# Kernel optimization log

Measured on AMD Instinct MI355X. Metric: run time of the kernel, lower is better.

## Reference

```python
import math
import jax, jax.numpy as jnp
import numpy as np

MODEL_DIM = 4096
NUM_EXPERTS = 16
COMP_PER_EXP = 4
PROJ_DIM = 4
TOTAL_COMP = NUM_EXPERTS * COMP_PER_EXP
B = 8192
K = 2
CAPACITY_FACTOR = 1.0
MIN_CAPACITY = 8
LOG2PI = math.log(2.0 * math.pi)


def setup_inputs() -> dict:
    key = jax.random.key(0)
    ks = jax.random.split(key, 4)
    input = jax.random.normal(ks[0], (B, MODEL_DIM), dtype=jnp.float32)
    # drop_centers mask (bernoulli over uniform prior ~ 1/64 each); deterministic all-false here
    drop_mask = jnp.zeros((TOTAL_COMP,), dtype=bool)
    means = jax.random.normal(ks[1], (TOTAL_COMP, PROJ_DIM), dtype=jnp.float32) / math.sqrt(PROJ_DIM)
    log_vars = jnp.full((TOTAL_COMP, PROJ_DIM), 4.0, dtype=jnp.float32)
    mix_logits = jnp.zeros((TOTAL_COMP,), dtype=jnp.float32)
    W_down = jax.random.normal(ks[2], (MODEL_DIM, PROJ_DIM), dtype=jnp.float32) / math.sqrt(MODEL_DIM)
    W_up = jax.random.normal(ks[3], (PROJ_DIM, MODEL_DIM), dtype=jnp.float32) / math.sqrt(PROJ_DIM)
    return {"input": input, "drop_mask": drop_mask, "means": means, "log_vars": log_vars,
            "mix_logits": mix_logits, "W_down": W_down, "W_up": W_up}


def top2gating(logits, capacity_factor, min_capacity):
    S, E = logits.shape
    gates = jax.nn.softmax(logits, axis=1)
    org_gates = gates
    idx1 = jnp.argmax(gates, axis=1)
    mask1 = jax.nn.one_hot(idx1, E, dtype=jnp.int32)
    logits_ex1 = jnp.where(mask1.astype(bool), -jnp.inf, logits)
    idx2 = jnp.argmax(logits_ex1, axis=1)
    mask2 = jax.nn.one_hot(idx2, E, dtype=jnp.int32)
    loc1 = jnp.cumsum(mask1, axis=0) - 1
    loc2 = jnp.cumsum(mask2, axis=0) - 1 + jnp.sum(mask1, axis=0, keepdims=True)
    exp_counts = jnp.sum(mask1 + mask2, axis=0)
    # _capacity: ceil(tokens/experts * 2*cf), floored at min_capacity (static)
    capacity = max(int(math.ceil(S / E * capacity_factor * 2.0)), min_capacity)
    mask1 = mask1 * (loc1 < capacity).astype(jnp.int32)
    mask2 = mask2 * (loc2 < capacity).astype(jnp.int32)
    loc1_s = jnp.sum(loc1 * mask1, axis=1)
    loc2_s = jnp.sum(loc2 * mask2, axis=1)
    m1f = mask1.astype(gates.dtype)
    m2f = mask2.astype(gates.dtype)
    g1 = jnp.sum(gates * m1f, axis=1)
    g2 = jnp.sum(gates * m2f, axis=1)
    denom = jnp.maximum(g1 + g2, jnp.finfo(gates.dtype).eps)
    g1 = g1 / denom
    g2 = g2 / denom
    oh1 = jax.nn.one_hot(loc1_s, capacity, dtype=gates.dtype)  # [S, C]
    oh2 = jax.nn.one_hot(loc2_s, capacity, dtype=gates.dtype)
    combine = (jnp.einsum('s,se,sc->sec', g1, m1f, oh1)
               + jnp.einsum('s,se,sc->sec', g2, m2f, oh2))
    dispatch = combine.astype(bool)
    return combine, dispatch, exp_counts, org_gates


def reference(input, drop_mask, means, log_vars, mix_logits, W_down, W_up):
    x = jax.lax.stop_gradient(input)
    # Down_Projector: linear down / up with reconstruction loss
    proj = x @ W_down                      # [B, P]
    recon = proj @ W_up                    # [B, D]
    recover_loss = jnp.mean((recon - x) ** 2)
    z = jax.lax.stop_gradient(proj)        # projected_input.detach()
    # GMM component log-likelihoods (diagonal covariance)
    diff = z[:, None, :] - means[None, :, :]           # [B, TC, P]
    vars_ = jnp.exp(log_vars)                          # [TC, P]
    mdist = jnp.sum(diff * diff / (vars_ + 1e-6), axis=-1)  # [B, TC]
    log_det = jnp.sum(log_vars, axis=-1)               # [TC]
    comp_logits = -0.5 * (mdist + log_det + PROJ_DIM * LOG2PI)
    gmm_logits = comp_logits + jax.nn.log_softmax(mix_logits)[None, :]
    gmm_logits = jnp.where(drop_mask[None, :], -jnp.inf, gmm_logits)
    posterior = jax.nn.softmax(gmm_logits, axis=-1)
    expert_post = jnp.max(posterior.reshape(-1, NUM_EXPERTS, COMP_PER_EXP), axis=2)  # [B, E]
    nll = -jnp.mean(jax.scipy.special.logsumexp(gmm_logits, axis=1))
    # sum of rolls for k=2
    expert_logits = expert_post + jnp.roll(expert_post, 1, axis=-1)
    combine, dispatch, exp_counts, org_gates = top2gating(
        jax.lax.stop_gradient(expert_logits), CAPACITY_FACTOR, MIN_CAPACITY)
    return (nll + recover_loss, combine, dispatch, exp_counts, org_gates)
```

## Files before the change

kernel.cpp:

```cpp
#include <hip/hip_runtime.h>
#include <math.h>

#define NTOK 8192
#define MD   4096
#define NE   16
#define CAP  1024
static __device__ const float LOG2PI_F = 1.8378770664093453f;

typedef float vf4 __attribute__((ext_vector_type(4)));

#define OFF_COMB 1ull
#define OFF_DISP (OFF_COMB + (size_t)NTOK * NE * CAP)
#define OFF_CNT  (OFF_DISP + (size_t)NTOK * NE * CAP)
#define OFF_ORG  (OFF_CNT + NE)
#define FILL_FLOATS ((size_t)OFF_ORG)
#define FILL_F4     (FILL_FLOATS / 4)
#define FILL_TAIL   (FILL_F4 * 4)

#define NBLK     2048
#define TOKBLK   512
#define CHUNK_F4 16384ull
#define NCHUNK   ((int)((FILL_F4 + CHUNK_F4 - 1) / CHUNK_F4))

__global__ __launch_bounds__(256) void kfused(
    const float* __restrict__ x, const float* __restrict__ means,
    const float* __restrict__ logv, const float* __restrict__ mix,
    const float* __restrict__ Wd, const float* __restrict__ Wu,
    float* __restrict__ out,
    int* __restrict__ e1w, int* __restrict__ e2w,
    float* __restrict__ g1w, float* __restrict__ g2w,
    float* __restrict__ nllp, float* __restrict__ recp,
    float4* __restrict__ pw, int* __restrict__ qctr)
{
    const int b    = blockIdx.x;
    const int tid  = threadIdx.x;
    const int lane = tid & 63;
    const int wave = tid >> 6;

    if (b < TOKBLK) {
        float* org_out = out + OFF_ORG;
        float4 mu = *reinterpret_cast<const float4*>(means + lane * 4);
        float4 lv = *reinterpret_cast<const float4*>(logv + lane * 4);
        const float logdet = lv.x + lv.y + lv.z + lv.w;
        const float iv0 = 1.f / (expf(lv.x) + 1e-6f);
        const float iv1 = 1.f / (expf(lv.y) + 1e-6f);
        const float iv2 = 1.f / (expf(lv.z) + 1e-6f);
        const float iv3 = 1.f / (expf(lv.w) + 1e-6f);
        float mz = mix[lane];
        float mmax = mz;
#pragma unroll
        for (int m = 32; m; m >>= 1) mmax = fmaxf(mmax, __shfl_xor(mmax, m));
        float msum = expf(mz - mmax);
#pragma unroll
        for (int m = 32; m; m >>= 1) msum += __shfl_xor(msum, m);
        const float cbase = -0.5f * (logdet + 4.0f * LOG2PI_F)
                          + (mz - (mmax + logf(msum)));

        for (int rep = 0; rep < 4; ++rep) {
            const int t = (b * 4 + wave) * 4 + rep;
            const float* xrow = x + (size_t)t * MD;

            float p0 = 0.f, p1 = 0.f, p2 = 0.f, p3 = 0.f;
            float r0 = 0.f, r1 = 0.f, r2 = 0.f, r3 = 0.f;
            float xn = 0.f;
#pragma unroll 4
            for (int j = 0; j < 16; ++j) {
                const int d0 = (j * 64 + lane) * 4;
                float4 v = *reinterpret_cast<const float4*>(xrow + d0);
                float4 w0 = *reinterpret_cast<const float4*>(Wd + (size_t)d0 * 4);
                float4 w1 = *reinterpret_cast<const float4*>(Wd + (size_t)(d0 + 1) * 4);
                float4 w2 = *reinterpret_cast<const float4*>(Wd + (size_t)(d0 + 2) * 4);
                float4 w3 = *reinterpret_cast<const float4*>(Wd + (size_t)(d0 + 3) * 4);
                p0 += v.x * w0.x + v.y * w1.x + v.z * w2.x + v.w * w3.x;
                p1 += v.x * w0.y + v.y * w1.y + v.z * w2.y + v.w * w3.y;
                p2 += v.x * w0.z + v.y * w1.z + v.z * w2.z + v.w * w3.z;
                p3 += v.x * w0.w + v.y * w1.w + v.z * w2.w + v.w * w3.w;
                float4 u0 = *reinterpret_cast<const float4*>(Wu + d0);
                float4 u1 = *reinterpret_cast<const float4*>(Wu + MD + d0);
                float4 u2 = *reinterpret_cast<const float4*>(Wu + 2 * MD + d0);
                float4 u3 = *reinterpret_cast<const float4*>(Wu + 3 * MD + d0);
                r0 += v.x * u0.x + v.y * u0.y + v.z * u0.z + v.w * u0.w;
                r1 += v.x * u1.x + v.y * u1.y + v.z * u1.z + v.w * u1.w;
                r2 += v.x * u2.x + v.y * u2.y + v.z * u2.z + v.w * u2.w;
                r3 += v.x * u3.x + v.y * u3.y + v.z * u3.z + v.w * u3.w;
                xn += v.x * v.x + v.y * v.y + v.z * v.z + v.w * v.w;
            }
#pragma unroll
            for (int m = 32; m; m >>= 1) {
                p0 += __shfl_xor(p0, m); p1 += __shfl_xor(p1, m);
                p2 += __shfl_xor(p2, m); p3 += __shfl_xor(p3, m);
                r0 += __shfl_xor(r0, m); r1 += __shfl_xor(r1, m);
                r2 += __shfl_xor(r2, m); r3 += __shfl_xor(r3, m);
                xn += __shfl_xor(xn, m);
            }

            if (lane == 0) {
                recp[t] = xn - 2.f * (p0 * r0 + p1 * r1 + p2 * r2 + p3 * r3);
                float4 pv; pv.x = p0; pv.y = p1; pv.z = p2; pv.w = p3;
                pw[t] = pv;
            }

            float dd, mdist;
            dd = p0 - mu.x; mdist  = dd * dd * iv0;
            dd = p1 - mu.y; mdist += dd * dd * iv1;
            dd = p2 - mu.z; mdist += dd * dd * iv2;
            dd = p3 - mu.w; mdist += dd * dd * iv3;
            float gl = -0.5f * mdist + cbase;

            float gmax = gl;
#pragma unroll
            for (int m = 32; m; m >>= 1) gmax = fmaxf(gmax, __shfl_xor(gmax, m));
            float gsum = expf(gl - gmax);
#pragma unroll
            for (int m = 32; m; m >>= 1) gsum += __shfl_xor(gsum, m);
            float lse = gmax + logf(gsum);
            if (lane == 0) nllp[t] = lse;
            float post = expf(gl - lse);

            float q = post;
            q = fmaxf(q, __shfl_xor(q, 1));
            q = fmaxf(q, __shfl_xor(q, 2));
            float ep = __shfl(q, (lane * 4) & 63);
            float epm1 = __shfl(ep, (lane + 15) & 15);
            float el = ep + epm1;

            float m16 = el;
#pragma unroll
            for (int m = 8; m; m >>= 1) m16 = fmaxf(m16, __shfl_xor(m16, m, 16));
            float ex = expf(el - m16);
            float s16 = ex;
#pragma unroll
            for (int m = 8; m; m >>= 1) s16 += __shfl_xor(s16, m, 16);
            float gate = ex / s16;

            float bv = gate; int bi = lane & 15;
#pragma unroll
            for (int m = 8; m; m >>= 1) {
                float ov = __shfl_xor(bv, m, 16); int oi = __shfl_xor(bi, m, 16);
                if (ov > bv || (ov == bv && oi < bi)) { bv = ov; bi = oi; }
            }
            int i1 = bi;
            float el2 = ((lane & 15) == i1) ? -INFINITY : el;
            float bv2 = el2; int bi2 = lane & 15;
#pragma unroll
            for (int m = 8; m; m >>= 1) {
                float ov = __shfl_xor(bv2, m, 16); int oi = __shfl_xor(bi2, m, 16);
                if (ov > bv2 || (ov == bv2 && oi < bi2)) { bv2 = ov; bi2 = oi; }
            }
            int i2 = bi2;
            float g1 = __shfl(gate, i1, 16);
            float g2 = __shfl(gate, i2, 16);

            if (lane < 16) org_out[(size_t)t * 16 + lane] = gate;
            if (lane == 0) { e1w[t] = i1; e2w[t] = i2; g1w[t] = g1; g2w[t] = g2; }
        }
    }

    {
        vf4 z = (vf4)(0.f);
        vf4* o4 = reinterpret_cast<vf4*>(out);
        for (;;) {
            int c = atomicAdd(qctr, 1);
            if (c >= NCHUNK) break;
            size_t base = (size_t)c * CHUNK_F4;
            size_t end  = base + CHUNK_F4;
            if (end > FILL_F4) end = FILL_F4;
            for (size_t i = base + tid; i < end; i += 256)
                __builtin_nontemporal_store(z, o4 + i);
        }
    }
    if (b == 0 && tid == 0) out[FILL_TAIL] = 0.f;
}

__global__ __launch_bounds__(256) void krank(
    const int* __restrict__ e1, const int* __restrict__ e2,
    int* __restrict__ loc1, int* __restrict__ rank2,
    int* __restrict__ cnt1, int* __restrict__ cnt2)
{
    const int e = blockIdx.x & 15;
    const bool second = blockIdx.x >= 16;
    const int* keys = second ? e2 : e1;
    int* outloc = second ? rank2 : loc1;
    __shared__ int wtot[4];
    const int tid = threadIdx.x;
    const int w = tid >> 6, l = tid & 63;

    int kreg[32];
#pragma unroll
    for (int k = 0; k < 32; ++k) kreg[k] = keys[k * 256 + tid];

    int running = 0;
#pragma unroll
    for (int k = 0; k < 32; ++k) {
        bool pred = (kreg[k] == e);
        unsigned long long mask = __ballot(pred);
        int rin = __popcll(mask & ((1ull << l) - 1ull));
        if (l == 0) wtot[w] = __popcll(mask);
        __syncthreads();
        int off = 0;
        for (int i = 0; i < w; ++i) off += wtot[i];
        if (pred) outloc[k * 256 + tid] = running + off + rin;
        running += wtot[0] + wtot[1] + wtot[2] + wtot[3];
        __syncthreads();
    }
    if (tid == 0) { if (second) cnt2[e] = running; else cnt1[e] = running; }
}

__global__ __launch_bounds__(256) void kfinal(
    const int* __restrict__ e1w, const int* __restrict__ e2w,
    const float* __restrict__ g1w, const float* __restrict__ g2w,
    const int* __restrict__ loc1w, const int* __restrict__ rank2w,
    const int* __restrict__ cnt1, const int* __restrict__ cnt2,
    const float* __restrict__ nllp, const float* __restrict__ recp,
    const float4* __restrict__ pw, const float* __restrict__ Wu,
    float* __restrict__ out)
{
    if (blockIdx.x == 32) {
        const int tid = threadIdx.x;
        const int w = tid >> 6, lane = tid & 63;
        float v[22];
#pragma unroll
        for (int q = 0; q < 22; ++q) v[q] = 0.f;
        for (int t = tid; t < NTOK; t += 256) {
            v[0] += nllp[t];
            v[1] += recp[t];
            float4 p = pw[t];
            v[2] += p.x * p.x; v[3] += p.x * p.y; v[4] += p.x * p.z; v[5] += p.x * p.w;
            v[6] += p.y * p.y; v[7] += p.y * p.z; v[8] += p.y * p.w;
            v[9] += p.z * p.z; v[10] += p.z * p.w; v[11] += p.w * p.w;
        }
        for (int d = tid; d < MD; d += 256) {
            float u0 = Wu[d], u1 = Wu[MD + d], u2 = Wu[2 * MD + d], u3 = Wu[3 * MD + d];
            v[12] += u0 * u0; v[13] += u0 * u1; v[14] += u0 * u2; v[15] += u0 * u3;
            v[16] += u1 * u1; v[17] += u1 * u2; v[18] += u1 * u3;
            v[19] += u2 * u2; v[20] += u2 * u3; v[21] += u3 * u3;
        }
        __shared__ float part[22][4];
#pragma unroll
        for (int q = 0; q < 22; ++q) {
            float s = v[q];
#pragma unroll
            for (int m = 32; m; m >>= 1) s += __shfl_xor(s, m);
            if (lane == 0) part[q][w] = s;
        }
        __syncthreads();
        if (tid == 0) {
            float r[22];
#pragma unroll
            for (int q = 0; q < 22; ++q)
                r[q] = part[q][0] + part[q][1] + part[q][2] + part[q][3];
            float gs = r[2] * r[12] + r[6] * r[16] + r[9] * r[19] + r[11] * r[21]
                     + 2.f * (r[3] * r[13] + r[4] * r[14] + r[5] * r[15]
                            + r[7] * r[17] + r[8] * r[18] + r[10] * r[20]);
            out[0] = (-r[0] / (float)NTOK)
                   + (r[1] + gs) / ((float)NTOK * (float)MD);
        }
        return;
    }

    if (blockIdx.x == 0 && threadIdx.x < NE)
        out[OFF_CNT + threadIdx.x] = (float)(cnt1[threadIdx.x] + cnt2[threadIdx.x]);

    const int t = blockIdx.x * 256 + threadIdx.x;
    const int e1 = e1w[t], e2 = e2w[t];
    const int l1 = loc1w[t];
    const int l2 = rank2w[t] + cnt1[e2];
    float g1 = g1w[t], g2 = g2w[t];
    const bool m1 = l1 < CAP, m2 = l2 < CAP;
    g1 = m1 ? g1 : 0.f;
    g2 = m2 ? g2 : 0.f;
    float denom = fmaxf(g1 + g2, 1.1920929e-07f);
    g1 /= denom; g2 /= denom;
    float* comb = out + OFF_COMB;
    float* disp = out + OFF_DISP;
    if (m1) {
        size_t idx = (size_t)t * (NE * CAP) + (size_t)e1 * CAP + l1;
        comb[idx] = g1;
        disp[idx] = (g1 != 0.f) ? 1.f : 0.f;
    }
    if (m2) {
        size_t idx = (size_t)t * (NE * CAP) + (size_t)e2 * CAP + l2;
        comb[idx] = g2;
        disp[idx] = (g2 != 0.f) ? 1.f : 0.f;
    }
}

extern "C" void kernel_launch(void* const* d_in, const int* in_sizes, int n_in,
                              void* d_out, int out_size, void* d_ws, size_t ws_size,
                              hipStream_t stream) {
    const float* x     = (const float*)d_in[0];
    const float* means = (const float*)d_in[2];
    const float* logv  = (const float*)d_in[3];
    const float* mix   = (const float*)d_in[4];
    const float* Wd    = (const float*)d_in[5];
    const float* Wu    = (const float*)d_in[6];
    float* out = (float*)d_out;

    int*   qctr  = (int*)d_ws;
    int*   e1w   = qctr + 4;
    int*   e2w   = e1w + NTOK;
    float* g1w   = (float*)(e2w + NTOK);
    float* g2w   = g1w + NTOK;
    int*   loc1  = (int*)(g2w + NTOK);
    int*   rank2 = loc1 + NTOK;
    int*   cnt1  = rank2 + NTOK;
    int*   cnt2  = cnt1 + NE;
    float* nllp  = (float*)(cnt2 + NE);
    float* recp  = nllp + NTOK;
    float4* pw   = (float4*)(recp + NTOK);

    hipMemsetAsync(qctr, 0, sizeof(int), stream);
    kfused<<<NBLK, 256, 0, stream>>>(x, means, logv, mix, Wd, Wu, out,
                                     e1w, e2w, g1w, g2w, nllp, recp, pw, qctr);
    krank<<<32, 256, 0, stream>>>(e1w, e2w, loc1, rank2, cnt1, cnt2);
    kfinal<<<33, 256, 0, stream>>>(e1w, e2w, g1w, g2w, loc1, rank2, cnt1, cnt2,
                                   nllp, recp, pw, Wu, out);
}
```

Measured before the change: 192.1 us.

## Overlap part of the zero-fill with the rank kernel to hide its latency

The large zero-fill of the combine and dispatch outputs is split in two. Most of it stays in the fused gating kernel, and a reserved 64 MiB tail is cleared by extra blocks added to the rank kernel, so that fill overlaps the serial 32-block ranking work that would otherwise leave the GPU mostly idle. The fill chunk size is also halved for finer load balancing. This costs one extra counter and more blocks in the rank launch, and those blocks compete for bandwidth with the ranking blocks.

```diff
diff --git a/kernel.cpp b/kernel.cpp
--- a/kernel.cpp
+++ b/kernel.cpp
@@ -17,10 +17,14 @@
 #define FILL_F4     (FILL_FLOATS / 4)
 #define FILL_TAIL   (FILL_F4 * 4)
 
+#define RESERVE_F4  4194304ull
+#define MAIN_F4     (FILL_F4 - RESERVE_F4)
+
 #define NBLK     2048
 #define TOKBLK   512
-#define CHUNK_F4 16384ull
-#define NCHUNK   ((int)((FILL_F4 + CHUNK_F4 - 1) / CHUNK_F4))
+#define CHUNK_F4 8192ull
+#define NCHUNK_MAIN ((int)((MAIN_F4 + CHUNK_F4 - 1) / CHUNK_F4))
+#define NCHUNK_RES  ((int)(RESERVE_F4 / CHUNK_F4))
 
 __global__ __launch_bounds__(256) void kfused(
     const float* __restrict__ x, const float* __restrict__ means,
@@ -161,28 +165,44 @@
         vf4* o4 = reinterpret_cast<vf4*>(out);
         for (;;) {
             int c = atomicAdd(qctr, 1);
-            if (c >= NCHUNK) break;
+            if (c >= NCHUNK_MAIN) break;
             size_t base = (size_t)c * CHUNK_F4;
+            size_t end  = base + CHUNK_F4;
+            if (end > MAIN_F4) end = MAIN_F4;
+            for (size_t i = base + tid; i < end; i += 256)
+                __builtin_nontemporal_store(z, o4 + i);
+        }
+    }
+    if (b == 0 && tid == 0) out[FILL_TAIL] = 0.f;
+}
+
+__global__ __launch_bounds__(256) void krank2(
+    const int* __restrict__ e1, const int* __restrict__ e2,
+    int* __restrict__ loc1, int* __restrict__ rank2,
+    int* __restrict__ cnt1, int* __restrict__ cnt2,
+    float* __restrict__ out, int* __restrict__ qctr2)
+{
+    const int tid = threadIdx.x;
+    if (blockIdx.x >= 32) {
+        vf4 z = (vf4)(0.f);
+        vf4* o4 = reinterpret_cast<vf4*>(out);
+        for (;;) {
+            int c = atomicAdd(qctr2, 1);
+            if (c >= NCHUNK_RES) break;
+            size_t base = MAIN_F4 + (size_t)c * CHUNK_F4;
             size_t end  = base + CHUNK_F4;
             if (end > FILL_F4) end = FILL_F4;
             for (size_t i = base + tid; i < end; i += 256)
                 __builtin_nontemporal_store(z, o4 + i);
         }
-    }
-    if (b == 0 && tid == 0) out[FILL_TAIL] = 0.f;
-}
-
-__global__ __launch_bounds__(256) void krank(
-    const int* __restrict__ e1, const int* __restrict__ e2,
-    int* __restrict__ loc1, int* __restrict__ rank2,
-    int* __restrict__ cnt1, int* __restrict__ cnt2)
-{
+        return;
+    }
+
     const int e = blockIdx.x & 15;
     const bool second = blockIdx.x >= 16;
     const int* keys = second ? e2 : e1;
     int* outloc = second ? rank2 : loc1;
     __shared__ int wtot[4];
-    const int tid = threadIdx.x;
     const int w = tid >> 6, l = tid & 63;
 
     int kreg[32];
@@ -309,10 +329,11 @@
     float* recp  = nllp + NTOK;
     float4* pw   = (float4*)(recp + NTOK);
 
-    hipMemsetAsync(qctr, 0, sizeof(int), stream);
+    hipMemsetAsync(qctr, 0, 2 * sizeof(int), stream);
     kfused<<<NBLK, 256, 0, stream>>>(x, means, logv, mix, Wd, Wu, out,
                                      e1w, e2w, g1w, g2w, nllp, recp, pw, qctr);
-    krank<<<32, 256, 0, stream>>>(e1w, e2w, loc1, rank2, cnt1, cnt2);
+    krank2<<<1024, 256, 0, stream>>>(e1w, e2w, loc1, rank2, cnt1, cnt2,
+                                     out, qctr + 1);
     kfinal<<<33, 256, 0, stream>>>(e1w, e2w, g1w, g2w, loc1, rank2, cnt1, cnt2,
                                    nllp, recp, pw, Wu, out);
 }
```

After: 236.0 us. 1.23x slower.
